# Kernel optimization log

Hardware: AMD Instinct MI355X
Metric: run time of the kernel (lower is better)

The kernel has to match this reference:

```python
import jax, jax.numpy as jnp
import numpy as np

B, L, H, N, NB = 16, 4096, 256, 64, 4
EXPAND = 2


def setup_inputs() -> dict:
    key = jax.random.key(0)
    ks = jax.random.split(key, 12)
    def nrm(k, shape, scale):
        return jax.random.normal(k, shape, dtype=jnp.float32) * scale
    inp = {}
    inp["x"] = jax.random.normal(ks[0], (B, L, 1), dtype=jnp.float32)
    # conv stem: Conv1d(1 -> H, kernel 5, pad 2)
    inp["conv_w"] = nrm(ks[1], (H, 1, 5), 1.0 / np.sqrt(5.0))
    inp["conv_b"] = jnp.zeros((H,), jnp.float32)
    # per-block S4 (S4D diagonal kernel) params, stacked over NB blocks
    inp["s4_norm_w"] = jnp.ones((NB, H), jnp.float32)
    inp["s4_norm_b"] = jnp.zeros((NB, H), jnp.float32)
    inp["log_dt"] = (np.log(0.001) + jax.random.uniform(ks[2], (NB, H), dtype=jnp.float32) * (np.log(0.1) - np.log(0.001))).astype(jnp.float32)
    inp["log_A_real"] = jnp.full((NB, H, N), np.log(0.5), jnp.float32)
    inp["A_imag"] = jnp.tile(np.pi * jnp.arange(N, dtype=jnp.float32), (NB, H, 1))
    inp["C_re"] = nrm(ks[3], (NB, H, N), 0.5 ** 0.5)
    inp["C_im"] = nrm(ks[4], (NB, H, N), 0.5 ** 0.5)
    inp["D"] = nrm(ks[5], (NB, H), 1.0)
    # S4 output GLU linear: H -> 2H, then glu -> H
    inp["s4_out_w"] = nrm(ks[6], (NB, 2 * H, H), 1.0 / np.sqrt(H))
    inp["s4_out_b"] = jnp.zeros((NB, 2 * H), jnp.float32)
    # FF block (expand=2)
    inp["ff_norm_w"] = jnp.ones((NB, H), jnp.float32)
    inp["ff_norm_b"] = jnp.zeros((NB, H), jnp.float32)
    inp["ff_w1"] = nrm(ks[7], (NB, EXPAND * H, H), 1.0 / np.sqrt(H))
    inp["ff_b1"] = jnp.zeros((NB, EXPAND * H), jnp.float32)
    inp["ff_w2"] = nrm(ks[8], (NB, H, EXPAND * H), 1.0 / np.sqrt(EXPAND * H))
    inp["ff_b2"] = jnp.zeros((NB, H), jnp.float32)
    return inp


def _ln_ch(x, w, b):
    # LayerNorm over channel dim of x: [B, H, L] (prenorm on transposed layout)
    mu = jnp.mean(x, axis=1, keepdims=True)
    var = jnp.mean((x - mu) ** 2, axis=1, keepdims=True)
    return (x - mu) * jax.lax.rsqrt(var + 1e-5) * w[None, :, None] + b[None, :, None]


def _s4d_kernel(log_dt, log_A_real, A_imag, C_re, C_im, Lk):
    # Diagonal SSM (S4D) convolution kernel, returns [H, Lk]
    dt = jnp.exp(log_dt)                       # [H]
    A = -jnp.exp(log_A_real) + 1j * A_imag     # [H, N]
    dtA = A * dt[:, None]                      # [H, N]
    C = (C_re + 1j * C_im) * (jnp.exp(dtA) - 1.0) / A
    V = jnp.exp(dtA[:, :, None] * jnp.arange(Lk, dtype=jnp.float32))  # [H, N, Lk]
    return 2.0 * jnp.einsum('hn,hnl->hl', C, V).real


def reference(x, conv_w, conv_b, s4_norm_w, s4_norm_b, log_dt, log_A_real, A_imag,
              C_re, C_im, D, s4_out_w, s4_out_b, ff_norm_w, ff_norm_b,
              ff_w1, ff_b1, ff_w2, ff_b2):
    u = jnp.transpose(x, (0, 2, 1))  # [B, 1, L]
    h = jax.lax.conv_general_dilated(u, conv_w, (1,), [(2, 2)],
                                     dimension_numbers=('NCH', 'OIH', 'NCH'))
    h = h + conv_b[None, :, None]    # [B, H, L]
    Lx = h.shape[-1]
    for i in range(NB):
        # --- S4 residual block (prenorm, FFT long conv, D-skip, GELU, GLU out) ---
        z = _ln_ch(h, s4_norm_w[i], s4_norm_b[i])
        k = _s4d_kernel(log_dt[i], log_A_real[i], A_imag[i], C_re[i], C_im[i], Lx)
        zf = jnp.fft.rfft(z, n=2 * Lx)
        kf = jnp.fft.rfft(k, n=2 * Lx)
        y = jnp.fft.irfft(zf * kf[None], n=2 * Lx)[..., :Lx]
        y = y + z * D[i][None, :, None]
        y = jax.nn.gelu(y, approximate=False)
        y2 = jnp.einsum('fh,bhl->bfl', s4_out_w[i], y) + s4_out_b[i][None, :, None]
        a, g = jnp.split(y2, 2, axis=1)
        h = h + a * jax.nn.sigmoid(g)
        # --- FF residual block (prenorm, pointwise MLP expand=2, GELU) ---
        z = _ln_ch(h, ff_norm_w[i], ff_norm_b[i])
        z = jax.nn.gelu(jnp.einsum('fh,bhl->bfl', ff_w1[i], z) + ff_b1[i][None, :, None], approximate=False)
        z = jnp.einsum('hf,bfl->bhl', ff_w2[i], z) + ff_b2[i][None, :, None]
        h = h + z
    return h[:, :, -1]  # [B, H]
```

## Files before the change

### kernel.cpp

```cpp
#include <hip/hip_runtime.h>
#include <math.h>

#define Bq 16
#define Lq 4096
#define Hq 256
#define Nq 64
#define NBq 4
#define F2q 512
#define BLq (Bq*Lq)

typedef __attribute__((ext_vector_type(8))) short short8;
typedef __attribute__((ext_vector_type(4))) float f32x4;

__device__ __forceinline__ unsigned short f2bf(float f){
  unsigned u = __float_as_uint(f);
  u = (u + 0x7fffu + ((u >> 16) & 1u)) >> 16;
  return (unsigned short)u;
}
__device__ __forceinline__ float bf2f(unsigned short u){
  return __uint_as_float(((unsigned)u) << 16);
}
__device__ __forceinline__ float gelu(float x){
  float u = 0.79788456f*x*(1.f + 0.044715f*x*x);
  float t = 1.f - __fdividef(2.f, 1.f + __expf(2.f*fabsf(u)));
  return 0.5f*x*(1.f + copysignf(t, u));
}

__device__ __forceinline__ void stage16(const void* g, void* l){
  __builtin_amdgcn_global_load_lds((const __attribute__((address_space(1))) void*)g,
                                   (__attribute__((address_space(3))) void*)l, 16, 0, 0);
}

__global__ __launch_bounds__(256) void k_convln(const float* __restrict__ x,
    const float* __restrict__ cw, const float* __restrict__ cb,
    unsigned short* __restrict__ h, float* __restrict__ mu, float* __restrict__ rstd){
  __shared__ float xs[260];
  __shared__ float cwS[Hq*5];
  __shared__ float cbS[Hq];
  const int b = blockIdx.x >> 4;
  const int l0 = (blockIdx.x & 15) * 256;
  const int tid = threadIdx.x;
  for (int i=tid; i<Hq*5; i+=256) cwS[i] = cw[i];
  cbS[tid] = cb[tid];
  {
    int gl = l0 + tid - 2;
    xs[tid] = (gl>=0 && gl<Lq) ? x[(size_t)b*Lq + gl] : 0.f;
    if (tid < 4){
      int gl2 = l0 + 254 + tid;
      xs[256+tid] = (gl2>=0 && gl2<Lq) ? x[(size_t)b*Lq + gl2] : 0.f;
    }
  }
  __syncthreads();
  float s0=0.f, s1=0.f;
  unsigned short* hp = h + (size_t)b*Hq*Lq + l0 + tid;
  for (int c=0;c<Hq;c++){
    float acc = cbS[c];
    #pragma unroll
    for (int k=0;k<5;k++) acc = fmaf(cwS[c*5+k], xs[tid+k], acc);
    hp[(size_t)c*Lq] = f2bf(acc);
    s0 += acc; s1 = fmaf(acc, acc, s1);
  }
  int col = b*Lq + l0 + tid;
  float m = s0 * (1.0f/256.0f);
  float var = s1*(1.0f/256.0f) - m*m;
  mu[col] = m;
  rstd[col] = rsqrtf(fmaxf(var, 0.f) + 1e-5f);
}

__global__ __launch_bounds__(256) void k_s4pre(const float* __restrict__ log_dt,
    const float* __restrict__ lar, const float* __restrict__ aim,
    const float* __restrict__ cre, const float* __restrict__ cim,
    float* __restrict__ wre, float* __restrict__ wim,
    float* __restrict__ c2re, float* __restrict__ c2im){
  int idx = blockIdx.x*256 + threadIdx.x;
  int hh = (idx >> 6) & (Hq-1);
  int i = idx >> 14;
  float dt = expf(log_dt[i*Hq + hh]);
  float are = -expf(lar[idx]);
  float ai  = aim[idx];
  float dre = are*dt, dim = ai*dt;
  float er = expf(dre);
  float wr = er*cosf(dim), wi = er*sinf(dim);
  float nr = wr - 1.f, ni = wi;
  float den = are*are + ai*ai;
  float qre = (nr*are + ni*ai)/den;
  float qim = (ni*are - nr*ai)/den;
  float Cr = cre[idx], Ci = cim[idx];
  float cer = Cr*qre - Ci*qim;
  float cei = Cr*qim + Ci*qre;
  wre[idx] = wr; wim[idx] = wi;
  c2re[idx] = 2.f*cer; c2im[idx] = 2.f*cei;
}

__global__ __launch_bounds__(256) void k_cvtw(const float* __restrict__ s0,
    const float* __restrict__ s1, const float* __restrict__ s2,
    unsigned short* __restrict__ d0, unsigned short* __restrict__ d1,
    unsigned short* __restrict__ d2){
  int idx = blockIdx.x*256 + threadIdx.x;
  d0[idx] = f2bf(s0[idx]);
  d1[idx] = f2bf(s1[idx]);
  d2[idx] = f2bf(s2[idx]);
}

__global__ __launch_bounds__(64) void k_s4mat(const float* __restrict__ wre_,
    const float* __restrict__ wim_, const float* __restrict__ c2re_,
    const float* __restrict__ c2im_, const float* __restrict__ Dp,
    unsigned short* __restrict__ G, unsigned short* __restrict__ Wb,
    float* __restrict__ w64re_, float* __restrict__ w64im_){
  __shared__ float Kv[64];
  const int n = threadIdx.x;
  const int ch = blockIdx.x;
  const int pidx = ch*64 + n;
  const float wr = wre_[pidx], wi = wim_[pidx];
  const float cr = c2re_[pidx], ci = c2im_[pidx];
  unsigned short* Gb = G + (size_t)ch*64*192;
  unsigned short* Wbb = Wb + (size_t)ch*128*64;
  float pre = 1.f, pim = 0.f;
  for (int t=0;t<64;t++){
    float a = cr*pre - ci*pim;
    #pragma unroll
    for (int m=1;m<64;m<<=1) a += __shfl_xor(a, m, 64);
    if (n==0) Kv[t] = a;
    Wbb[n*64 + (63-t)] = f2bf(pre);
    Wbb[(64+n)*64 + (63-t)] = f2bf(pim);
    float qre = pre*wr - pim*wi;
    float qim = pre*wi + pim*wr;
    Gb[t*192 + 64 + n]  = f2bf(cr*qre - ci*qim);
    Gb[t*192 + 128 + n] = f2bf(-(cr*qim + ci*qre));
    pre = qre; pim = qim;
  }
  w64re_[pidx] = pre; w64im_[pidx] = pim;
  __syncthreads();
  float dv = Dp[ch];
  for (int t=0;t<64;t++){
    float kv = (n<=t) ? Kv[t-n] : 0.f;
    if (n==t) kv += dv;
    Gb[t*192 + n] = f2bf(kv);
  }
}

__global__ __launch_bounds__(256) void k_lnfin(const float2* __restrict__ stats,
    float* __restrict__ mu, float* __restrict__ rstd){
  int col = blockIdx.x*256 + threadIdx.x;
  float2 s = stats[col];
  float m = s.x * (1.0f/256.0f);
  float var = s.y*(1.0f/256.0f) - m*m;
  mu[col] = m;
  rstd[col] = rsqrtf(fmaxf(var, 0.f) + 1e-5f);
}

__global__ __launch_bounds__(256) void k_prep(const unsigned short* __restrict__ h,
    const float* __restrict__ mu, const float* __restrict__ rstd,
    const float* __restrict__ lnw_, const float* __restrict__ lnb_,
    unsigned short* __restrict__ U, int ib){
  int idx = blockIdx.x*256 + threadIdx.x;
  int l = (idx & 511) * 8;
  int ch = (idx >> 9) & (Hq-1);
  int b = idx >> 17;
  float lw = lnw_[ib*Hq+ch], lb = lnb_[ib*Hq+ch];
  const unsigned short* hp = h + (((size_t)(b*Hq+ch))<<12) + l;
  const float* mp = mu + ((size_t)b<<12) + l;
  const float* rp = rstd + ((size_t)b<<12) + l;
  uint4 hv = *(const uint4*)hp;
  float hf[8];
  hf[0]=bf2f(hv.x&0xffff); hf[1]=bf2f(hv.x>>16);
  hf[2]=bf2f(hv.y&0xffff); hf[3]=bf2f(hv.y>>16);
  hf[4]=bf2f(hv.z&0xffff); hf[5]=bf2f(hv.z>>16);
  hf[6]=bf2f(hv.w&0xffff); hf[7]=bf2f(hv.w>>16);
  unsigned ow[8];
  #pragma unroll
  for (int j=0;j<8;j++){
    float z = (hf[j]-mp[j])*rp[j]*lw + lb;
    ow[j] = f2bf(z);
  }
  uint4 o;
  o.x = ow[0] | (ow[1]<<16); o.y = ow[2] | (ow[3]<<16);
  o.z = ow[4] | (ow[5]<<16); o.w = ow[6] | (ow[7]<<16);
  unsigned short* up = U + ((size_t)ch*1024 + b*64 + (l>>6))*192 + (l&63);
  *(uint4*)up = o;
}

__global__ __launch_bounds__(256,2) void k_bgemm(const unsigned short* __restrict__ Wb,
    const unsigned short* __restrict__ U, unsigned short* __restrict__ Bb){
  __shared__ __align__(16) char smem[34816];
  unsigned short* Alds = (unsigned short*)smem;
  unsigned short* Blds = (unsigned short*)(smem+16384);
  const int tid = threadIdx.x;
  const int lam = tid & 63;
  const int wv = tid >> 6;
  const int wr = wv >> 1, wc = wv & 1;
  const int ch = blockIdx.x;
  const int bc0 = blockIdx.y * 128;
  const unsigned short* Wch = Wb + (size_t)ch*128*64;
  const unsigned short* Uch = U + (size_t)ch*1024*192;
  const int rbase = lam & 15;
  const int kg = lam >> 4;
  const int x7 = lam & 7;
  const int xo0 = ((kg) ^ x7) * 8;
  const int xo1 = ((4+kg) ^ x7) * 8;
  f32x4 acc[4][4] = {};
  #pragma unroll
  for (int c=0;c<4;c++){
    int si = c*256 + tid;
    int row = si >> 3, blk = si & 7;
    int sb = blk ^ (row & 7);
    stage16(Wch + row*64 + sb*8, &Alds[(c*256 + wv*64)*8]);
    stage16(Uch + (size_t)(bc0+row)*192 + sb*8, &Blds[(c*256 + wv*64)*8]);
  }
  __syncthreads();
  #pragma unroll
  for (int kk=0;kk<2;kk++){
    const int xo = kk ? xo1 : xo0;
    short8 af[4], wf[4];
    #pragma unroll
    for (int mf=0;mf<4;mf++)
      af[mf] = *(const short8*)&Alds[(wr*64 + mf*16 + rbase)*64 + xo];
    #pragma unroll
    for (int nf=0;nf<4;nf++)
      wf[nf] = *(const short8*)&Blds[(wc*64 + nf*16 + rbase)*64 + xo];
    #pragma unroll
    for (int mf=0;mf<4;mf++)
      #pragma unroll
      for (int nf=0;nf<4;nf++)
        acc[mf][nf] = __builtin_amdgcn_mfma_f32_16x16x32_bf16(af[mf], wf[nf], acc[mf][nf], 0,0,0);
  }
  __syncthreads();
  unsigned* tru = (unsigned*)smem;
  const int mg = lam >> 4;
  const int ncol = lam & 15;
  #pragma unroll
  for (int nf=0;nf<4;nf++){
    int bcl = wc*64 + nf*16 + ncol;
    #pragma unroll
    for (int mf=0;mf<4;mf++){
      int n2h = wr*32 + mf*8 + mg*2;
      tru[bcl*68 + n2h]     = (unsigned)f2bf(acc[mf][nf][0]) | ((unsigned)f2bf(acc[mf][nf][1])<<16);
      tru[bcl*68 + n2h + 1] = (unsigned)f2bf(acc[mf][nf][2]) | ((unsigned)f2bf(acc[mf][nf][3])<<16);
    }
  }
  __syncthreads();
  {
    int row = tid >> 1, half = tid & 1;
    const unsigned* src = tru + row*68 + half*32;
    unsigned short* dst = Bb + ((size_t)ch*1024 + bc0 + row)*128 + half*64;
    #pragma unroll
    for (int j=0;j<8;j++)
      *(uint4*)(dst + j*8) = *(const uint4*)(src + j*4);
  }
}

__global__ __launch_bounds__(256) void k_cscan(const unsigned short* __restrict__ Bb,
    const float* __restrict__ w64re_, const float* __restrict__ w64im_,
    unsigned short* __restrict__ U){
  const int wid = blockIdx.x*4 + (threadIdx.x >> 6);
  const int n = threadIdx.x & 63;
  const int ch = wid & (Hq-1);
  const int b = wid >> 8;
  const float wr = w64re_[ch*64 + n];
  const float wi = w64im_[ch*64 + n];
  const unsigned short* bp = Bb + ((size_t)ch*1024 + b*64)*128 + n;
  unsigned short* up = U + ((size_t)ch*1024 + b*64)*192;
  float sre = 0.f, sim = 0.f;
  for (int c=0;c<64;c++){
    up[c*192 + 64 + n]  = f2bf(sre);
    up[c*192 + 128 + n] = f2bf(sim);
    float br = bf2f(bp[c*128]), bi = bf2f(bp[c*128 + 64]);
    float t = fmaf(wr, sre, fmaf(-wi, sim, br));
    sim = fmaf(wr, sim, fmaf(wi, sre, bi));
    sre = t;
  }
}

__global__ __launch_bounds__(256,2) void k_ygemm(const unsigned short* __restrict__ G,
    const unsigned short* __restrict__ U, unsigned short* __restrict__ ybuf){
  __shared__ __align__(16) char smem[40960];
  unsigned short* Alds = (unsigned short*)smem;
  unsigned short* Blds = (unsigned short*)(smem + 8192);
  const int tid = threadIdx.x;
  const int lam = tid & 63;
  const int wv = tid >> 6;
  const int ch = blockIdx.x;
  const int col0 = blockIdx.y * 256;
  const unsigned short* Gch = G + (size_t)ch*64*192;
  const unsigned short* Uch = U + (size_t)ch*1024*192;
  const int rbase = lam & 15;
  const int kg = lam >> 4;
  const int x7 = lam & 7;
  const int xo0 = ((kg) ^ x7) * 8;
  const int xo1 = ((4+kg) ^ x7) * 8;
  f32x4 acc[4][4] = {};
  for (int ks=0;ks<3;ks++){
    const int k0 = ks*64;
    #pragma unroll
    for (int c=0;c<2;c++){
      int si = c*256 + tid;
      int row = si >> 3, blk = si & 7;
      int sb = blk ^ (row & 7);
      stage16(Gch + row*192 + k0 + sb*8, &Alds[(c*256 + wv*64)*8]);
    }
    #pragma unroll
    for (int c=0;c<8;c++){
      int si = c*256 + tid;
      int row = si >> 3, blk = si & 7;
      int sb = blk ^ (row & 7);
      stage16(Uch + (size_t)(col0+row)*192 + k0 + sb*8, &Blds[(c*256 + wv*64)*8]);
    }
    __syncthreads();
    #pragma unroll
    for (int kk=0;kk<2;kk++){
      const int xo = kk ? xo1 : xo0;
      short8 af[4], wf[4];
      #pragma unroll
      for (int mf=0;mf<4;mf++)
        af[mf] = *(const short8*)&Alds[(mf*16 + rbase)*64 + xo];
      #pragma unroll
      for (int nf=0;nf<4;nf++)
        wf[nf] = *(const short8*)&Blds[(wv*64 + nf*16 + rbase)*64 + xo];
      #pragma unroll
      for (int mf=0;mf<4;mf++)
        #pragma unroll
        for (int nf=0;nf<4;nf++)
          acc[mf][nf] = __builtin_amdgcn_mfma_f32_16x16x32_bf16(af[mf], wf[nf], acc[mf][nf], 0,0,0);
    }
    __syncthreads();
  }
  unsigned short* trans = (unsigned short*)smem + wv*64*66;
  const int mg = lam >> 4;
  const int ncol = lam & 15;
  #pragma unroll
  for (int mf=0;mf<4;mf++){
    #pragma unroll
    for (int nf=0;nf<4;nf++){
      #pragma unroll
      for (int r=0;r<4;r++){
        int l = mf*16 + mg*4 + r;
        int bcl = nf*16 + ncol;
        trans[bcl*66 + l] = f2bf(gelu(acc[mf][nf][r]));
      }
    }
  }
  __syncthreads();
  const int bc = col0 + wv*64 + lam;
  const int b = bc >> 6, c = bc & 63;
  unsigned short* yp = ybuf + (((size_t)(b*Hq + ch))<<12) + c*64;
  #pragma unroll
  for (int j=0;j<8;j++){
    uint4 v = *(const uint4*)&trans[lam*66 + j*8];
    *(uint4*)(yp + j*8) = v;
  }
}

__global__ __launch_bounds__(256) void k_transp(const unsigned short* __restrict__ src,
    unsigned short* __restrict__ dst){
  __shared__ unsigned lds[64][65];
  const int t = threadIdx.x;
  const int tile = blockIdx.x;
  const int l0 = (tile & 63)*64;
  const int c0 = ((tile>>6)&3)*64;
  const int b = tile >> 8;
  const int rr = t >> 3, c8 = t & 7;
  #pragma unroll
  for (int q=0;q<2;q++){
    int ch = rr + q*32;
    const unsigned short* sp = src + ((size_t)b*Hq + c0+ch)*Lq + l0 + c8*8;
    uint4 v = *(const uint4*)sp;
    lds[ch][c8*8+0] = v.x & 0xffff; lds[ch][c8*8+1] = v.x >> 16;
    lds[ch][c8*8+2] = v.y & 0xffff; lds[ch][c8*8+3] = v.y >> 16;
    lds[ch][c8*8+4] = v.z & 0xffff; lds[ch][c8*8+5] = v.z >> 16;
    lds[ch][c8*8+6] = v.w & 0xffff; lds[ch][c8*8+7] = v.w >> 16;
  }
  __syncthreads();
  #pragma unroll
  for (int q=0;q<2;q++){
    int l = rr + q*32;
    unsigned a[8];
    #pragma unroll
    for (int j=0;j<8;j++) a[j] = lds[c8*8+j][l];
    uint4 o;
    o.x = (a[0]&0xffff) | (a[1]<<16);
    o.y = (a[2]&0xffff) | (a[3]<<16);
    o.z = (a[4]&0xffff) | (a[5]<<16);
    o.w = (a[6]&0xffff) | (a[7]<<16);
    *(uint4*)(dst + ((size_t)b*Lq + l0+l)*Hq + c0 + c8*8) = o;
  }
}

__global__ __launch_bounds__(256) void k_lntransp(const unsigned short* __restrict__ h,
    const float* __restrict__ mu, const float* __restrict__ rstd,
    const float* __restrict__ lnw_, const float* __restrict__ lnb_,
    unsigned short* __restrict__ dst, int ib){
  __shared__ unsigned lds[64][65];
  const int t = threadIdx.x;
  const int tile = blockIdx.x;
  const int l0 = (tile & 63)*64;
  const int c0 = ((tile>>6)&3)*64;
  const int b = tile >> 8;
  const int rr = t >> 3, c8 = t & 7;
  #pragma unroll
  for (int q=0;q<2;q++){
    int ch = c0 + rr + q*32;
    float lw = lnw_[ib*Hq + ch], lb = lnb_[ib*Hq + ch];
    const unsigned short* sp = h + ((size_t)b*Hq + ch)*Lq + l0 + c8*8;
    const float* mp = mu + (size_t)b*Lq + l0 + c8*8;
    const float* rp = rstd + (size_t)b*Lq + l0 + c8*8;
    uint4 hv = *(const uint4*)sp;
    float hf[8];
    hf[0]=bf2f(hv.x&0xffff); hf[1]=bf2f(hv.x>>16);
    hf[2]=bf2f(hv.y&0xffff); hf[3]=bf2f(hv.y>>16);
    hf[4]=bf2f(hv.z&0xffff); hf[5]=bf2f(hv.z>>16);
    hf[6]=bf2f(hv.w&0xffff); hf[7]=bf2f(hv.w>>16);
    #pragma unroll
    for (int j=0;j<8;j++){
      float z = (hf[j] - mp[j]) * rp[j] * lw + lb;
      lds[rr + q*32][c8*8+j] = f2bf(z);
    }
  }
  __syncthreads();
  #pragma unroll
  for (int q=0;q<2;q++){
    int l = rr + q*32;
    unsigned a[8];
    #pragma unroll
    for (int j=0;j<8;j++) a[j] = lds[c8*8+j][l];
    uint4 o;
    o.x = (a[0]&0xffff) | (a[1]<<16);
    o.y = (a[2]&0xffff) | (a[3]<<16);
    o.z = (a[4]&0xffff) | (a[5]<<16);
    o.w = (a[6]&0xffff) | (a[7]<<16);
    *(uint4*)(dst + ((size_t)b*Lq + l0+l)*Hq + c0 + c8*8) = o;
  }
}

template<int MODE, int KDIM>
__global__ __launch_bounds__(256,2) void k_gemm(
    const unsigned short* __restrict__ A, const unsigned short* __restrict__ W,
    const float* __restrict__ bias, unsigned short* __restrict__ h,
    unsigned short* __restrict__ out, float2* __restrict__ stats){
  constexpr int WSH = (MODE==0?2:1)*128*64;
  constexpr int STG_B = (128*64 + WSH)*2;
  constexpr int EPI_B = (MODE==1) ? 128*136*2 : 64*144*4;
  constexpr int SMEM = STG_B > EPI_B ? STG_B : EPI_B;
  __shared__ __align__(16) char smem[SMEM];
  unsigned short* Alds = (unsigned short*)smem;
  unsigned short* Wlds = Alds + 128*64;
  const int tid = threadIdx.x;
  const int lam = tid & 63;
  const int wv = tid >> 6;
  const int wr = wv >> 1, wc = wv & 1;
  const int col0 = blockIdx.x * 128;
  const int n0 = blockIdx.y * 128;
  const int rbase = lam & 15;
  const int kg = lam >> 4;
  const int x7 = lam & 7;
  const int xo0 = ((kg) ^ x7) * 8;
  const int xo1 = ((4+kg) ^ x7) * 8;
  const unsigned short *aP[4], *wP[4], *wP2[4];
  unsigned sDst[4];
  #pragma unroll
  for (int c=0;c<4;c++){
    int si = c*256 + tid;
    int row = si >> 3, blk = si & 7;
    int sb = blk ^ (row & 7);
    aP[c] = A + (size_t)(col0+row)*KDIM + sb*8;
    wP[c] = W + (size_t)(n0+row)*KDIM + sb*8;
    wP2[c] = (MODE==0) ? (W + (size_t)(n0+256+row)*KDIM + sb*8) : nullptr;
    sDst[c] = (unsigned)(c*256 + wv*64)*8;
  }
  f32x4 acc[4][4] = {};
  f32x4 acc2[4][(MODE==0)?4:1] = {};
  for (int k0 = 0; k0 < KDIM; k0 += 64){
    #pragma unroll
    for (int c=0;c<4;c++){
      stage16(aP[c] + k0, &Alds[sDst[c]]);
      stage16(wP[c] + k0, &Wlds[sDst[c]]);
      if constexpr (MODE==0) stage16(wP2[c] + k0, &Wlds[8192 + sDst[c]]);
    }
    __syncthreads();
    #pragma unroll
    for (int kk=0;kk<2;kk++){
      const int xo = kk ? xo1 : xo0;
      short8 af[4], wf[4];
      #pragma unroll
      for (int mf=0;mf<4;mf++)
        af[mf] = *(const short8*)&Alds[(wr*64 + mf*16 + rbase)*64 + xo];
      #pragma unroll
      for (int nf=0;nf<4;nf++)
        wf[nf] = *(const short8*)&Wlds[(wc*64 + nf*16 + rbase)*64 + xo];
      if constexpr (MODE==0){
        short8 wg[4];
        #pragma unroll
        for (int nf=0;nf<4;nf++)
          wg[nf] = *(const short8*)&Wlds[8192 + (wc*64 + nf*16 + rbase)*64 + xo];
        #pragma unroll
        for (int mf=0;mf<4;mf++){
          #pragma unroll
          for (int nf=0;nf<4;nf++){
            acc[mf][nf]  = __builtin_amdgcn_mfma_f32_16x16x32_bf16(af[mf], wf[nf], acc[mf][nf], 0,0,0);
            acc2[mf][nf] = __builtin_amdgcn_mfma_f32_16x16x32_bf16(af[mf], wg[nf], acc2[mf][nf], 0,0,0);
          }
        }
      } else {
        #pragma unroll
        for (int mf=0;mf<4;mf++){
          #pragma unroll
          for (int nf=0;nf<4;nf++)
            acc[mf][nf] = __builtin_amdgcn_mfma_f32_16x16x32_bf16(af[mf], wf[nf], acc[mf][nf], 0,0,0);
        }
      }
    }
    __syncthreads();
  }
  const int mg = lam >> 4;
  const int ncol = lam & 15;
  if constexpr (MODE==1){
    unsigned short* trans = (unsigned short*)smem;
    #pragma unroll
    for (int nf=0;nf<4;nf++){
      int gnl = wc*64 + nf*16 + ncol;
      float bb1 = bias[n0 + gnl];
      #pragma unroll
      for (int mf=0;mf<4;mf++){
        int cl = wr*64 + mf*16 + mg*4;
        #pragma unroll
        for (int r=0;r<4;r++)
          trans[(cl+r)*136 + gnl] = f2bf(gelu(acc[mf][nf][r] + bb1));
      }
    }
    __syncthreads();
    {
      int cl = tid >> 1, gs = (tid & 1)*64;
      const unsigned short* src = trans + cl*136 + gs;
      unsigned short* dst = out + (size_t)(col0+cl)*F2q + n0 + gs;
      #pragma unroll
      for (int j=0;j<8;j++)
        *(uint4*)(dst + j*8) = *(const uint4*)(src + j*8);
    }
  } else {
    float* dlds = (float*)smem;
    const int bb = col0 >> 12;
    const int l0 = col0 & (Lq-1);
    #pragma unroll
    for (int p=0;p<2;p++){
      __syncthreads();
      if (wc == p){
        #pragma unroll
        for (int nf=0;nf<4;nf++){
          int chl = nf*16 + ncol;
          int gn = n0 + p*64 + chl;
          float ba = bias[gn];
          float bg = (MODE==0) ? bias[gn + Hq] : 0.f;
          #pragma unroll
          for (int mf=0;mf<4;mf++){
            int coll = wr*64 + mf*16 + mg*4;
            f32x4 dv;
            #pragma unroll
            for (int r=0;r<4;r++){
              if constexpr (MODE==0){
                float av = acc[mf][nf][r] + ba;
                float gv = acc2[mf][nf][r] + bg;
                dv[r] = __fdividef(av, 1.f + __expf(-gv));
              } else {
                dv[r] = acc[mf][nf][r] + ba;
              }
            }
            *(f32x4*)&dlds[chl*144 + (coll>>5)*36 + (coll&31)] = dv;
          }
        }
      }
      __syncthreads();
      {
        int chl = tid >> 2, seg = tid & 3;
        unsigned short* hp = h + ((size_t)bb*Hq + n0 + p*64 + chl)*Lq + l0 + seg*32;
        float* dp = dlds + chl*144 + seg*36;
        #pragma unroll
        for (int j=0;j<4;j++){
          uint4 hv = *(uint4*)(hp + j*8);
          f32x4 d0 = *(const f32x4*)(dp + j*8);
          f32x4 d1 = *(const f32x4*)(dp + j*8 + 4);
          d0[0] += bf2f(hv.x&0xffff); d0[1] += bf2f(hv.x>>16);
          d0[2] += bf2f(hv.y&0xffff); d0[3] += bf2f(hv.y>>16);
          d1[0] += bf2f(hv.z&0xffff); d1[1] += bf2f(hv.z>>16);
          d1[2] += bf2f(hv.w&0xffff); d1[3] += bf2f(hv.w>>16);
          hv.x = (unsigned)f2bf(d0[0]) | ((unsigned)f2bf(d0[1])<<16);
          hv.y = (unsigned)f2bf(d0[2]) | ((unsigned)f2bf(d0[3])<<16);
          hv.z = (unsigned)f2bf(d1[0]) | ((unsigned)f2bf(d1[1])<<16);
          hv.w = (unsigned)f2bf(d1[2]) | ((unsigned)f2bf(d1[3])<<16);
          *(uint4*)(hp + j*8) = hv;
          *(f32x4*)(dp + j*8) = d0;
          *(f32x4*)(dp + j*8 + 4) = d1;
        }
      }
      __syncthreads();
      {
        int j = tid >> 1, hc = (tid & 1)*32;
        int js = (j>>5)*36 + (j&31);
        float s0 = 0.f, s1 = 0.f;
        #pragma unroll
        for (int c=0;c<32;c++){
          float v = dlds[(hc+c)*144 + js];
          s0 += v; s1 = fmaf(v, v, s1);
        }
        s0 += __shfl_xor(s0, 1, 64);
        s1 += __shfl_xor(s1, 1, 64);
        if (!(tid & 1)){
          atomicAdd(&stats[col0 + j].x, s0);
          atomicAdd(&stats[col0 + j].y, s1);
        }
      }
    }
  }
}

__global__ __launch_bounds__(256) void k_gather(const unsigned short* __restrict__ h,
    float* __restrict__ o){
  int idx = blockIdx.x*256 + threadIdx.x;
  int b = idx >> 8, c = idx & (Hq-1);
  o[idx] = bf2f(h[((size_t)b*Hq + c)*Lq + (Lq-1)]);
}

extern "C" void kernel_launch(void* const* d_in, const int* in_sizes, int n_in,
                              void* d_out, int out_size, void* d_ws, size_t ws_size,
                              hipStream_t stream) {
  (void)in_sizes; (void)n_in; (void)out_size; (void)ws_size;
  const float* x         = (const float*)d_in[0];
  const float* conv_w    = (const float*)d_in[1];
  const float* conv_b    = (const float*)d_in[2];
  const float* s4_norm_w = (const float*)d_in[3];
  const float* s4_norm_b = (const float*)d_in[4];
  const float* log_dt    = (const float*)d_in[5];
  const float* log_A_real= (const float*)d_in[6];
  const float* A_imag    = (const float*)d_in[7];
  const float* C_re      = (const float*)d_in[8];
  const float* C_im      = (const float*)d_in[9];
  const float* Dp        = (const float*)d_in[10];
  const float* s4_out_w  = (const float*)d_in[11];
  const float* s4_out_b  = (const float*)d_in[12];
  const float* ff_norm_w = (const float*)d_in[13];
  const float* ff_norm_b = (const float*)d_in[14];
  const float* ff_w1     = (const float*)d_in[15];
  const float* ff_b1     = (const float*)d_in[16];
  const float* ff_w2     = (const float*)d_in[17];
  const float* ff_b2     = (const float*)d_in[18];

  char* ws = (char*)d_ws;
  size_t off = 0;
  auto nxt = [&](size_t bytes){ size_t o = off; off = (off + bytes + 255) & ~(size_t)255; return o; };
  unsigned short* h = (unsigned short*)(ws + nxt((size_t)Bq*Hq*Lq*2));
  float* mu     = (float*)(ws + nxt((size_t)BLq*4));
  float* rstd   = (float*)(ws + nxt((size_t)BLq*4));
  float* wre    = (float*)(ws + nxt((size_t)NBq*Hq*Nq*4));
  float* wim    = (float*)(ws + nxt((size_t)NBq*Hq*Nq*4));
  float* c2re   = (float*)(ws + nxt((size_t)NBq*Hq*Nq*4));
  float* c2im   = (float*)(ws + nxt((size_t)NBq*Hq*Nq*4));
  float* w64re  = (float*)(ws + nxt((size_t)NBq*Hq*Nq*4));
  float* w64im  = (float*)(ws + nxt((size_t)NBq*Hq*Nq*4));
  unsigned short* s4wb = (unsigned short*)(ws + nxt((size_t)NBq*F2q*Hq*2));
  unsigned short* f1b  = (unsigned short*)(ws + nxt((size_t)NBq*F2q*Hq*2));
  unsigned short* f2b  = (unsigned short*)(ws + nxt((size_t)NBq*Hq*F2q*2));
  unsigned short* Gm   = (unsigned short*)(ws + nxt((size_t)Hq*64*192*2));
  unsigned short* Wbar = (unsigned short*)(ws + nxt((size_t)Hq*128*64*2));
  unsigned short* U    = (unsigned short*)(ws + nxt((size_t)Hq*1024*192*2));
  unsigned short* Bb   = (unsigned short*)(ws + nxt((size_t)Hq*128*1024*2));
  unsigned short* ybuf = Bb;
  unsigned short* yT   = Bb + (size_t)16*1024*1024;
  unsigned short* zT   = yT;
  unsigned short* z2T  = U;
  float2* stats = (float2*)Bb;

  k_convln<<<Bq*16, 256, 0, stream>>>(x, conv_w, conv_b, h, mu, rstd);
  k_s4pre<<<(NBq*Hq*Nq)/256, 256, 0, stream>>>(log_dt, log_A_real, A_imag, C_re, C_im,
                                               wre, wim, c2re, c2im);
  k_cvtw<<<(NBq*F2q*Hq)/256, 256, 0, stream>>>(s4_out_w, ff_w1, ff_w2, s4wb, f1b, f2b);

  for (int i=0;i<NBq;i++){
    const size_t po = (size_t)i*Hq*Nq;
    k_s4mat<<<Hq, 64, 0, stream>>>(wre+po, wim+po, c2re+po, c2im+po, Dp + i*Hq,
                                   Gm, Wbar, w64re+po, w64im+po);
    k_prep<<<(Bq*Hq*Lq/8)/256, 256, 0, stream>>>(h, mu, rstd, s4_norm_w, s4_norm_b, U, i);
    k_bgemm<<<dim3(Hq, 8), 256, 0, stream>>>(Wbar, U, Bb);
    k_cscan<<<(Bq*Hq)/4, 256, 0, stream>>>(Bb, w64re+po, w64im+po, U);
    k_ygemm<<<dim3(Hq, 4), 256, 0, stream>>>(Gm, U, ybuf);
    k_transp<<<Bq*4*64, 256, 0, stream>>>(ybuf, yT);
    hipMemsetAsync(stats, 0, (size_t)BLq*sizeof(float2), stream);
    k_gemm<0,256><<<dim3(BLq/128, 2), 256, 0, stream>>>(
        yT, s4wb + (size_t)i*F2q*Hq, s4_out_b + (size_t)i*F2q, h, nullptr, stats);
    k_lnfin<<<BLq/256, 256, 0, stream>>>(stats, mu, rstd);
    k_lntransp<<<Bq*4*64, 256, 0, stream>>>(h, mu, rstd, ff_norm_w, ff_norm_b, zT, i);
    k_gemm<1,256><<<dim3(BLq/128, 4), 256, 0, stream>>>(
        zT, f1b + (size_t)i*F2q*Hq, ff_b1 + (size_t)i*F2q, nullptr, z2T, nullptr);
    hipMemsetAsync(stats, 0, (size_t)BLq*sizeof(float2), stream);
    k_gemm<2,512><<<dim3(BLq/128, 2), 256, 0, stream>>>(
        z2T, f2b + (size_t)i*Hq*F2q, ff_b2 + (size_t)i*Hq, h, nullptr, stats);
    k_lnfin<<<BLq/256, 256, 0, stream>>>(stats, mu, rstd);
  }
  k_gather<<<(Bq*Hq)/256, 256, 0, stream>>>(h, (float*)d_out);
}
```

Before: 1.212 ms.

## Replace atomic LayerNorm stats with per-tile partial sums and double-buffer GEMM staging

The residual GEMM epilogues no longer use atomicAdd into a zeroed stats buffer. Each blockIdx.y half now writes its own partial sum and sum-of-squares into a separate buffer (st0, st1). The consuming kernels (prep, lntransp) combine the two partials and compute mean and rstd inline, which removes the memsets, the k_lnfin launches and the atomic traffic. Separately, the MODE 1 and MODE 2 GEMMs get ping-pong double-buffered LDS staging so global-to-LDS loads overlap with MFMA work. The cost is that shared memory for those GEMMs grows to 64KB, which can lower occupancy, and the stats are now recomputed redundantly per element in the consumer kernels.

```diff
diff --git a/kernel.cpp b/kernel.cpp
--- a/kernel.cpp
+++ b/kernel.cpp
@@ -25,6 +25,11 @@
   float t = 1.f - __fdividef(2.f, 1.f + __expf(2.f*fabsf(u)));
   return 0.5f*x*(1.f + copysignf(t, u));
 }
+__device__ __forceinline__ float2 lnstat(float2 a, float2 b){
+  float m = (a.x + b.x) * (1.0f/256.0f);
+  float var = (a.y + b.y)*(1.0f/256.0f) - m*m;
+  return make_float2(m, rsqrtf(fmaxf(var, 0.f) + 1e-5f));
+}
 
 __device__ __forceinline__ void stage16(const void* g, void* l){
   __builtin_amdgcn_global_load_lds((const __attribute__((address_space(1))) void*)g,
@@ -33,7 +38,7 @@
 
 __global__ __launch_bounds__(256) void k_convln(const float* __restrict__ x,
     const float* __restrict__ cw, const float* __restrict__ cb,
-    unsigned short* __restrict__ h, float* __restrict__ mu, float* __restrict__ rstd){
+    unsigned short* __restrict__ h, float2* __restrict__ st0, float2* __restrict__ st1){
   __shared__ float xs[260];
   __shared__ float cwS[Hq*5];
   __shared__ float cbS[Hq];
@@ -61,10 +66,8 @@
     s0 += acc; s1 = fmaf(acc, acc, s1);
   }
   int col = b*Lq + l0 + tid;
-  float m = s0 * (1.0f/256.0f);
-  float var = s1*(1.0f/256.0f) - m*m;
-  mu[col] = m;
-  rstd[col] = rsqrtf(fmaxf(var, 0.f) + 1e-5f);
+  st0[col] = make_float2(s0, s1);
+  st1[col] = make_float2(0.f, 0.f);
 }
 
 __global__ __launch_bounds__(256) void k_s4pre(const float* __restrict__ log_dt,
@@ -139,18 +142,8 @@
   }
 }
 
-__global__ __launch_bounds__(256) void k_lnfin(const float2* __restrict__ stats,
-    float* __restrict__ mu, float* __restrict__ rstd){
-  int col = blockIdx.x*256 + threadIdx.x;
-  float2 s = stats[col];
-  float m = s.x * (1.0f/256.0f);
-  float var = s.y*(1.0f/256.0f) - m*m;
-  mu[col] = m;
-  rstd[col] = rsqrtf(fmaxf(var, 0.f) + 1e-5f);
-}
-
 __global__ __launch_bounds__(256) void k_prep(const unsigned short* __restrict__ h,
-    const float* __restrict__ mu, const float* __restrict__ rstd,
+    const float2* __restrict__ st0, const float2* __restrict__ st1,
     const float* __restrict__ lnw_, const float* __restrict__ lnb_,
     unsigned short* __restrict__ U, int ib){
   int idx = blockIdx.x*256 + threadIdx.x;
@@ -159,8 +152,7 @@
   int b = idx >> 17;
   float lw = lnw_[ib*Hq+ch], lb = lnb_[ib*Hq+ch];
   const unsigned short* hp = h + (((size_t)(b*Hq+ch))<<12) + l;
-  const float* mp = mu + ((size_t)b<<12) + l;
-  const float* rp = rstd + ((size_t)b<<12) + l;
+  const int colb = (b<<12) + l;
   uint4 hv = *(const uint4*)hp;
   float hf[8];
   hf[0]=bf2f(hv.x&0xffff); hf[1]=bf2f(hv.x>>16);
@@ -170,7 +162,8 @@
   unsigned ow[8];
   #pragma unroll
   for (int j=0;j<8;j++){
-    float z = (hf[j]-mp[j])*rp[j]*lw + lb;
+    float2 mr = lnstat(st0[colb+j], st1[colb+j]);
+    float z = (hf[j]-mr.x)*mr.y*lw + lb;
     ow[j] = f2bf(z);
   }
   uint4 o;
@@ -386,7 +379,7 @@
 }
 
 __global__ __launch_bounds__(256) void k_lntransp(const unsigned short* __restrict__ h,
-    const float* __restrict__ mu, const float* __restrict__ rstd,
+    const float2* __restrict__ st0, const float2* __restrict__ st1,
     const float* __restrict__ lnw_, const float* __restrict__ lnb_,
     unsigned short* __restrict__ dst, int ib){
   __shared__ unsigned lds[64][65];
@@ -401,8 +394,7 @@
     int ch = c0 + rr + q*32;
     float lw = lnw_[ib*Hq + ch], lb = lnb_[ib*Hq + ch];
     const unsigned short* sp = h + ((size_t)b*Hq + ch)*Lq + l0 + c8*8;
-    const float* mp = mu + (size_t)b*Lq + l0 + c8*8;
-    const float* rp = rstd + (size_t)b*Lq + l0 + c8*8;
+    const int colb = b*Lq + l0 + c8*8;
     uint4 hv = *(const uint4*)sp;
     float hf[8];
     hf[0]=bf2f(hv.x&0xffff); hf[1]=bf2f(hv.x>>16);
@@ -411,7 +403,8 @@
     hf[6]=bf2f(hv.w&0xffff); hf[7]=bf2f(hv.w>>16);
     #pragma unroll
     for (int j=0;j<8;j++){
-      float z = (hf[j] - mp[j]) * rp[j] * lw + lb;
+      float2 mr = lnstat(st0[colb+j], st1[colb+j]);
+      float z = (hf[j] - mr.x) * mr.y * lw + lb;
       lds[rr + q*32][c8*8+j] = f2bf(z);
     }
   }
@@ -436,13 +429,12 @@
     const unsigned short* __restrict__ A, const unsigned short* __restrict__ W,
     const float* __restrict__ bias, unsigned short* __restrict__ h,
     unsigned short* __restrict__ out, float2* __restrict__ stats){
-  constexpr int WSH = (MODE==0?2:1)*128*64;
-  constexpr int STG_B = (128*64 + WSH)*2;
+  constexpr int NSTEP = KDIM/64;
+  constexpr int STG_B = (MODE==0) ? 49152 : 65536;
   constexpr int EPI_B = (MODE==1) ? 128*136*2 : 64*144*4;
   constexpr int SMEM = STG_B > EPI_B ? STG_B : EPI_B;
   __shared__ __align__(16) char smem[SMEM];
-  unsigned short* Alds = (unsigned short*)smem;
-  unsigned short* Wlds = Alds + 128*64;
+  unsigned short* S = (unsigned short*)smem;
   const int tid = threadIdx.x;
   const int lam = tid & 63;
   const int wv = tid >> 6;
@@ -468,29 +460,22 @@
   }
   f32x4 acc[4][4] = {};
   f32x4 acc2[4][(MODE==0)?4:1] = {};
-  for (int k0 = 0; k0 < KDIM; k0 += 64){
-    #pragma unroll
-    for (int c=0;c<4;c++){
-      stage16(aP[c] + k0, &Alds[sDst[c]]);
-      stage16(wP[c] + k0, &Wlds[sDst[c]]);
-      if constexpr (MODE==0) stage16(wP2[c] + k0, &Wlds[8192 + sDst[c]]);
-    }
-    __syncthreads();
+  auto MF = [&](const unsigned short* Ad, const unsigned short* Wd){
     #pragma unroll
     for (int kk=0;kk<2;kk++){
       const int xo = kk ? xo1 : xo0;
       short8 af[4], wf[4];
       #pragma unroll
       for (int mf=0;mf<4;mf++)
-        af[mf] = *(const short8*)&Alds[(wr*64 + mf*16 + rbase)*64 + xo];
+        af[mf] = *(const short8*)&Ad[(wr*64 + mf*16 + rbase)*64 + xo];
       #pragma unroll
       for (int nf=0;nf<4;nf++)
-        wf[nf] = *(const short8*)&Wlds[(wc*64 + nf*16 + rbase)*64 + xo];
+        wf[nf] = *(const short8*)&Wd[(wc*64 + nf*16 + rbase)*64 + xo];
       if constexpr (MODE==0){
         short8 wg[4];
         #pragma unroll
         for (int nf=0;nf<4;nf++)
-          wg[nf] = *(const short8*)&Wlds[8192 + (wc*64 + nf*16 + rbase)*64 + xo];
+          wg[nf] = *(const short8*)&Wd[8192 + (wc*64 + nf*16 + rbase)*64 + xo];
         #pragma unroll
         for (int mf=0;mf<4;mf++){
           #pragma unroll
@@ -508,12 +493,49 @@
         }
       }
     }
+  };
+  if constexpr (MODE==0){
+    unsigned short* Alds = S;
+    unsigned short* Wlds = S + 8192;
+    for (int k0 = 0; k0 < KDIM; k0 += 64){
+      #pragma unroll
+      for (int c=0;c<4;c++){
+        stage16(aP[c] + k0, &Alds[sDst[c]]);
+        stage16(wP[c] + k0, &Wlds[sDst[c]]);
+        stage16(wP2[c] + k0, &Wlds[8192 + sDst[c]]);
+      }
+      __syncthreads();
+      MF(Alds, Wlds);
+      __syncthreads();
+    }
+  } else {
+    unsigned short* A0 = S;            unsigned short* W0 = S + 8192;
+    unsigned short* A1 = S + 16384;    unsigned short* W1 = S + 24576;
+    auto STG = [&](unsigned short* Ad, unsigned short* Wd, int ko){
+      #pragma unroll
+      for (int c=0;c<4;c++){
+        stage16(aP[c] + ko, &Ad[sDst[c]]);
+        stage16(wP[c] + ko, &Wd[sDst[c]]);
+      }
+    };
+    STG(A0, W0, 0);
     __syncthreads();
+    #pragma unroll
+    for (int t=0; t<NSTEP; t+=2){
+      if (t+1 < NSTEP) STG(A1, W1, (t+1)*64);
+      MF(A0, W0);
+      __syncthreads();
+      if (t+1 < NSTEP){
+        if (t+2 < NSTEP) STG(A0, W0, (t+2)*64);
+        MF(A1, W1);
+        __syncthreads();
+      }
+    }
   }
   const int mg = lam >> 4;
   const int ncol = lam & 15;
   if constexpr (MODE==1){
-    unsigned short* trans = (unsigned short*)smem;
+    unsigned short* trans = S;
     #pragma unroll
     for (int nf=0;nf<4;nf++){
       int gnl = wc*64 + nf*16 + ncol;
@@ -539,6 +561,7 @@
     float* dlds = (float*)smem;
     const int bb = col0 >> 12;
     const int l0 = col0 & (Lq-1);
+    float s0t = 0.f, s1t = 0.f;
     #pragma unroll
     for (int p=0;p<2;p++){
       __syncthreads();
@@ -602,11 +625,12 @@
         }
         s0 += __shfl_xor(s0, 1, 64);
         s1 += __shfl_xor(s1, 1, 64);
-        if (!(tid & 1)){
-          atomicAdd(&stats[col0 + j].x, s0);
-          atomicAdd(&stats[col0 + j].y, s1);
-        }
-      }
+        s0t += s0; s1t += s1;
+      }
+    }
+    if (!(tid & 1)){
+      float2* stP = stats + (size_t)blockIdx.y*BLq;
+      stP[col0 + (tid >> 1)] = make_float2(s0t, s1t);
     }
   }
 }
@@ -646,8 +670,6 @@
   size_t off = 0;
   auto nxt = [&](size_t bytes){ size_t o = off; off = (off + bytes + 255) & ~(size_t)255; return o; };
   unsigned short* h = (unsigned short*)(ws + nxt((size_t)Bq*Hq*Lq*2));
-  float* mu     = (float*)(ws + nxt((size_t)BLq*4));
-  float* rstd   = (float*)(ws + nxt((size_t)BLq*4));
   float* wre    = (float*)(ws + nxt((size_t)NBq*Hq*Nq*4));
   float* wim    = (float*)(ws + nxt((size_t)NBq*Hq*Nq*4));
   float* c2re   = (float*)(ws + nxt((size_t)NBq*Hq*Nq*4));
@@ -665,9 +687,10 @@
   unsigned short* yT   = Bb + (size_t)16*1024*1024;
   unsigned short* zT   = yT;
   unsigned short* z2T  = U;
-  float2* stats = (float2*)Bb;
-
-  k_convln<<<Bq*16, 256, 0, stream>>>(x, conv_w, conv_b, h, mu, rstd);
+  float2* st0 = (float2*)Bb;
+  float2* st1 = st0 + BLq;
+
+  k_convln<<<Bq*16, 256, 0, stream>>>(x, conv_w, conv_b, h, st0, st1);
   k_s4pre<<<(NBq*Hq*Nq)/256, 256, 0, stream>>>(log_dt, log_A_real, A_imag, C_re, C_im,
                                                wre, wim, c2re, c2im);
   k_cvtw<<<(NBq*F2q*Hq)/256, 256, 0, stream>>>(s4_out_w, ff_w1, ff_w2, s4wb, f1b, f2b);
@@ -676,22 +699,18 @@
     const size_t po = (size_t)i*Hq*Nq;
     k_s4mat<<<Hq, 64, 0, stream>>>(wre+po, wim+po, c2re+po, c2im+po, Dp + i*Hq,
                                    Gm, Wbar, w64re+po, w64im+po);
-    k_prep<<<(Bq*Hq*Lq/8)/256, 256, 0, stream>>>(h, mu, rstd, s4_norm_w, s4_norm_b, U, i);
+    k_prep<<<(Bq*Hq*Lq/8)/256, 256, 0, stream>>>(h, st0, st1, s4_norm_w, s4_norm_b, U, i);
     k_bgemm<<<dim3(Hq, 8), 256, 0, stream>>>(Wbar, U, Bb);
     k_cscan<<<(Bq*Hq)/4, 256, 0, stream>>>(Bb, w64re+po, w64im+po, U);
     k_ygemm<<<dim3(Hq, 4), 256, 0, stream>>>(Gm, U, ybuf);
     k_transp<<<Bq*4*64, 256, 0, stream>>>(ybuf, yT);
-    hipMemsetAsync(stats, 0, (size_t)BLq*sizeof(float2), stream);
     k_gemm<0,256><<<dim3(BLq/128, 2), 256, 0, stream>>>(
-        yT, s4wb + (size_t)i*F2q*Hq, s4_out_b + (size_t)i*F2q, h, nullptr, stats);
-    k_lnfin<<<BLq/256, 256, 0, stream>>>(stats, mu, rstd);
-    k_lntransp<<<Bq*4*64, 256, 0, stream>>>(h, mu, rstd, ff_norm_w, ff_norm_b, zT, i);
+        yT, s4wb + (size_t)i*F2q*Hq, s4_out_b + (size_t)i*F2q, h, nullptr, st0);
+    k_lntransp<<<Bq*4*64, 256, 0, stream>>>(h, st0, st1, ff_norm_w, ff_norm_b, zT, i);
     k_gemm<1,256><<<dim3(BLq/128, 4), 256, 0, stream>>>(
         zT, f1b + (size_t)i*F2q*Hq, ff_b1 + (size_t)i*F2q, nullptr, z2T, nullptr);
-    hipMemsetAsync(stats, 0, (size_t)BLq*sizeof(float2), stream);
     k_gemm<2,512><<<dim3(BLq/128, 2), 256, 0, stream>>>(
-        z2T, f2b + (size_t)i*Hq*F2q, ff_b2 + (size_t)i*Hq, h, nullptr, stats);
-    k_lnfin<<<BLq/256, 256, 0, stream>>>(stats, mu, rstd);
+        z2T, f2b + (size_t)i*Hq*F2q, ff_b2 + (size_t)i*Hq, h, nullptr, st0);
   }
   k_gather<<<(Bq*Hq)/256, 256, 0, stream>>>(h, (float*)d_out);
 }
```

New measurement: 1.332 ms. 9.9% more time.
